# Kernel tuning notes

Measured on AMD Instinct MI355X. Metric: run time of the kernel, lower is better.

Reference implementation:

```python
import jax, jax.numpy as jnp
import numpy as np

N, E, D_IN, H, C = 50000, 1200000, 128, 8, 8  # heads=8, per-head dim=8, hidden=64
EPS_BN = 1e-5


def _bn(x, g, b):
    # BatchNorm1d in training mode: per-feature batch mean / biased var
    m = x.mean(0)
    v = x.var(0)
    return g * (x - m) * jax.lax.rsqrt(v + EPS_BN) + b


def _gatv2(x, src, dst, Wl, Wr, att):
    # PyG GATv2Conv (concat=True, bias=False, negative_slope=0.2, eval-mode dropout)
    xl = (x @ Wl).reshape(N, H, C)  # source transform (lin_l)
    xr = (x @ Wr).reshape(N, H, C)  # target transform (lin_r)
    e = jax.nn.leaky_relu(xl[src] + xr[dst], 0.2)          # [E,H,C]
    logits = jnp.einsum('ehc,hc->eh', e, att)               # [E,H]
    mx = jax.ops.segment_max(logits, dst, num_segments=N)   # [N,H]
    ex = jnp.exp(logits - mx[dst])
    den = jax.ops.segment_sum(ex, dst, num_segments=N)      # [N,H]
    alpha = ex / (den[dst] + 1e-16)                         # segment softmax over in-edges
    msg = xl[src] * alpha[..., None]                        # [E,H,C]
    out = jax.ops.segment_sum(msg.reshape(E, H * C), dst, num_segments=N)
    return out  # [N,64]


def setup_inputs() -> dict:
    key = jax.random.key(0)
    ks = jax.random.split(key, 40)
    d = {}
    d['x'] = jax.random.normal(ks[0], (N, D_IN), dtype=jnp.float32)
    d['edge_index'] = jax.random.randint(ks[1], (2, E), 0, N, dtype=jnp.int64)
    d['Wpre'] = jax.random.normal(ks[2], (D_IN, 64), dtype=jnp.float32) * 0.05
    d['g0'] = jnp.ones((64,), jnp.float32); d['b0'] = jnp.zeros((64,), jnp.float32)
    for i, k0 in zip(range(1, 5), range(3, 19, 4)):
        d[f'Wl{i}'] = jax.random.normal(ks[k0], (64, 64), jnp.float32) * 0.1
        d[f'Wr{i}'] = jax.random.normal(ks[k0 + 1], (64, 64), jnp.float32) * 0.1
        d[f'att{i}'] = jax.random.normal(ks[k0 + 2], (H, C), jnp.float32) * 0.1
        d[f'g{i}'] = jnp.ones((64,), jnp.float32)
        d[f'b{i}'] = jnp.zeros((64,), jnp.float32)
    dims = [64, 48, 32, 16, 2]
    for j in range(4):
        d[f'Wp{j+1}'] = jax.random.normal(ks[20 + j], (dims[j], dims[j + 1]), jnp.float32) * 0.1
        d[f'bp{j+1}'] = jnp.zeros((dims[j + 1],), jnp.float32)
    return d


def reference(x, edge_index, Wpre, g0, b0,
              Wl1, Wr1, att1, g1, b1,
              Wl2, Wr2, att2, g2, b2,
              Wl3, Wr3, att3, g3, b3,
              Wl4, Wr4, att4, g4, b4,
              Wp1, bp1, Wp2, bp2, Wp3, bp3, Wp4, bp4):
    src, dst = edge_index[0], edge_index[1]
    h = jax.nn.elu(_bn(x @ Wpre, g0, b0))
    for Wl, Wr, att, g, b in ((Wl1, Wr1, att1, g1, b1),
                              (Wl2, Wr2, att2, g2, b2),
                              (Wl3, Wr3, att3, g3, b3),
                              (Wl4, Wr4, att4, g4, b4)):
        h = jax.nn.elu(_bn(_gatv2(h, src, dst, Wl, Wr, att) + h, g, b))
    h = jax.nn.elu(h @ Wp1 + bp1)
    h = jax.nn.elu(h @ Wp2 + bp2)
    h = jax.nn.elu(h @ Wp3 + bp3)
    return h @ Wp4 + bp4
```

## Files before the change

### kernel.cpp

```cpp
#include <hip/hip_runtime.h>
#include <hip/hip_bf16.h>
#include <cmath>

__device__ inline void unpack_bf2(unsigned int u, float& lo, float& hi) {
    union { unsigned int i; float f; } a, b;
    a.i = u << 16; b.i = u & 0xffff0000u;
    lo = a.f; hi = b.f;
}
__device__ inline unsigned short bf16_bits(float x) {
    __hip_bfloat16 v = __float2bfloat16(x);
    return *reinterpret_cast<unsigned short*>(&v);
}

template<int K, int M, int ROWS>
__global__ __launch_bounds__(256)
void bn_gemm_kernel(const float* __restrict__ A, const float* __restrict__ B0,
                    const float* __restrict__ B1, float* __restrict__ C,
                    __hip_bfloat16* __restrict__ xlb, __hip_bfloat16* __restrict__ xrb,
                    const float* __restrict__ stats, const float* __restrict__ g,
                    const float* __restrict__ b, int N, float invN)
{
    constexpr int TM  = ROWS * M / 512;
    constexpr int LDA = K + 4;
    constexpr int MT  = M / TM;
    __shared__ float Bs[K * M];
    __shared__ float As[ROWS * LDA];
    __shared__ float sA[K], sB[K];
    if (stats != nullptr && threadIdx.x < K) {
        float m   = stats[threadIdx.x] * invN;
        float var = stats[K + threadIdx.x] * invN - m * m;
        float a   = g[threadIdx.x] * rsqrtf(var + 1e-5f);
        sA[threadIdx.x] = a;
        sB[threadIdx.x] = b[threadIdx.x] - m * a;
    }
    for (int i = threadIdx.x; i < K * M; i += 256) {
        float v;
        if (B1 != nullptr) {
            int k = i / M, m = i - k * M;
            v = (m < M / 2) ? B0[k * (M / 2) + m] : B1[k * (M / 2) + (m - M / 2)];
        } else {
            v = B0[i];
        }
        Bs[i] = v;
    }
    __syncthreads();
    int row0 = blockIdx.x * ROWS;
    for (int i = threadIdx.x; i < ROWS * K; i += 256) {
        int rr = i / K, kk = i - rr * K;
        int r = row0 + rr;
        float v = (r < N) ? A[(size_t)r * K + kk] : 0.f;
        if (stats != nullptr) {
            float t = fmaf(v, sA[kk], sB[kk]);
            v = (t > 0.f) ? t : expm1f(t);
        }
        As[rr * LDA + kk] = v;
    }
    __syncthreads();
    int r0 = (threadIdx.x / MT) * 2;
    int m0 = (threadIdx.x % MT) * TM;
    float acc0[TM], acc1[TM];
    #pragma unroll
    for (int i = 0; i < TM; ++i) { acc0[i] = 0.f; acc1[i] = 0.f; }
    const float* a0p = &As[r0 * LDA];
    const float* a1p = a0p + LDA;
    for (int k = 0; k < K; ++k) {
        float a0 = a0p[k], a1 = a1p[k];
        #pragma unroll
        for (int mm = 0; mm < TM; mm += 4) {
            float4 bv = *(const float4*)&Bs[k * M + m0 + mm];
            acc0[mm + 0] = fmaf(a0, bv.x, acc0[mm + 0]);
            acc0[mm + 1] = fmaf(a0, bv.y, acc0[mm + 1]);
            acc0[mm + 2] = fmaf(a0, bv.z, acc0[mm + 2]);
            acc0[mm + 3] = fmaf(a0, bv.w, acc0[mm + 3]);
            acc1[mm + 0] = fmaf(a1, bv.x, acc1[mm + 0]);
            acc1[mm + 1] = fmaf(a1, bv.y, acc1[mm + 1]);
            acc1[mm + 2] = fmaf(a1, bv.z, acc1[mm + 2]);
            acc1[mm + 3] = fmaf(a1, bv.w, acc1[mm + 3]);
        }
    }
    int rA = row0 + r0, rB = rA + 1;
    if (C != nullptr) {
        #pragma unroll
        for (int mm = 0; mm < TM; mm += 4) {
            if (rA < N)
                *(float4*)&C[(size_t)rA * M + m0 + mm] =
                    make_float4(acc0[mm], acc0[mm+1], acc0[mm+2], acc0[mm+3]);
            if (rB < N)
                *(float4*)&C[(size_t)rB * M + m0 + mm] =
                    make_float4(acc1[mm], acc1[mm+1], acc1[mm+2], acc1[mm+3]);
        }
    } else {
        unsigned int u0[4], u1[4];
        #pragma unroll
        for (int i = 0; i < 4; ++i) {
            u0[i] = (unsigned int)bf16_bits(acc0[2*i]) |
                    ((unsigned int)bf16_bits(acc0[2*i+1]) << 16);
            u1[i] = (unsigned int)bf16_bits(acc1[2*i]) |
                    ((unsigned int)bf16_bits(acc1[2*i+1]) << 16);
        }
        __hip_bfloat16* dst = (m0 < 64) ? xlb : xrb;
        int mo = (m0 < 64) ? m0 : m0 - 64;
        if (rA < N) *(uint4*)(dst + (size_t)rA * 64 + mo) = make_uint4(u0[0],u0[1],u0[2],u0[3]);
        if (rB < N) *(uint4*)(dst + (size_t)rB * 64 + mo) = make_uint4(u1[0],u1[1],u1[2],u1[3]);
    }
}

__global__ __launch_bounds__(256)
void bin_hist_kernel(const int* __restrict__ dsts, int* __restrict__ binCnt, int E)
{
    __shared__ int lh[256];
    lh[threadIdx.x] = 0;
    __syncthreads();
    for (int e = blockIdx.x * 256 + threadIdx.x; e < E; e += gridDim.x * 256)
        atomicAdd(&lh[dsts[e] >> 8], 1);
    __syncthreads();
    if (lh[threadIdx.x] > 0) atomicAdd(&binCnt[threadIdx.x], lh[threadIdx.x]);
}

__global__ __launch_bounds__(256)
void bin_scan_kernel(const int* __restrict__ binCnt, int* __restrict__ binBase,
                     int* __restrict__ binCursor, int* __restrict__ row_ptr,
                     int N, int E)
{
    __shared__ int buf[256];
    int v = binCnt[threadIdx.x];
    buf[threadIdx.x] = v;
    __syncthreads();
    for (int off = 1; off < 256; off <<= 1) {
        int t = (threadIdx.x >= off) ? buf[threadIdx.x - off] : 0;
        __syncthreads();
        buf[threadIdx.x] += t;
        __syncthreads();
    }
    int excl = buf[threadIdx.x] - v;
    binBase[threadIdx.x] = excl;
    binCursor[threadIdx.x] = excl;
    if (threadIdx.x == 255) {
        binBase[256] = buf[255];
        row_ptr[N] = E;
    }
}

#define SCHUNK 4096
__global__ __launch_bounds__(256)
void bin_scatter_kernel(const int* __restrict__ srcs, const int* __restrict__ dsts,
                        int* __restrict__ binCursor, int2* __restrict__ binned, int E)
{
    __shared__ int2 stg[SCHUNK];
    __shared__ int bcnt[256], bexcl[256], bcur[256], gbase[256], sbuf[256];
    int c0 = blockIdx.x * SCHUNK;
    int n = min(SCHUNK, E - c0);
    bcnt[threadIdx.x] = 0;
    __syncthreads();
    for (int k = 0; k < SCHUNK / 256; ++k) {
        int i = c0 + k * 256 + threadIdx.x;
        if (i < E) atomicAdd(&bcnt[dsts[i] >> 8], 1);
    }
    __syncthreads();
    int v = bcnt[threadIdx.x];
    sbuf[threadIdx.x] = v;
    __syncthreads();
    for (int off = 1; off < 256; off <<= 1) {
        int t = (threadIdx.x >= off) ? sbuf[threadIdx.x - off] : 0;
        __syncthreads();
        sbuf[threadIdx.x] += t;
        __syncthreads();
    }
    bexcl[threadIdx.x] = sbuf[threadIdx.x] - v;
    bcur[threadIdx.x]  = sbuf[threadIdx.x] - v;
    __syncthreads();
    for (int k = 0; k < SCHUNK / 256; ++k) {
        int i = c0 + k * 256 + threadIdx.x;
        if (i < E) {
            int s = srcs[i], d = dsts[i];
            int pos = atomicAdd(&bcur[d >> 8], 1);
            stg[pos] = make_int2(s, d);
        }
    }
    __syncthreads();
    gbase[threadIdx.x] = atomicAdd(&binCursor[threadIdx.x], bcnt[threadIdx.x]);
    __syncthreads();
    for (int i = threadIdx.x; i < n; i += 256) {
        int2 p = stg[i];
        int b = p.y >> 8;
        binned[gbase[b] + (i - bexcl[b])] = p;
    }
}

__global__ __launch_bounds__(256)
void bin_finalize_kernel(const int2* __restrict__ binned, const int* __restrict__ binBase,
                         int* __restrict__ row_ptr, int* __restrict__ col, int N)
{
    __shared__ int cnt[256], excl[256], cur[256];
    int b = blockIdx.x;
    int beg = binBase[b], end = binBase[b + 1];
    cnt[threadIdx.x] = 0;
    __syncthreads();
    for (int i = beg + threadIdx.x; i < end; i += 256)
        atomicAdd(&cnt[binned[i].y & 255], 1);
    __syncthreads();
    int v = cnt[threadIdx.x];
    excl[threadIdx.x] = v;
    __syncthreads();
    for (int off = 1; off < 256; off <<= 1) {
        int t = (threadIdx.x >= off) ? excl[threadIdx.x - off] : 0;
        __syncthreads();
        excl[threadIdx.x] += t;
        __syncthreads();
    }
    int ex = excl[threadIdx.x] - v;
    int dstIdx = b * 256 + threadIdx.x;
    if (dstIdx < N) row_ptr[dstIdx] = beg + ex;
    cur[threadIdx.x] = ex;
    __syncthreads();
    for (int i = beg + threadIdx.x; i < end; i += 256) {
        int2 p = binned[i];
        int pos = atomicAdd(&cur[p.y & 255], 1);
        col[beg + pos] = p.x << 7;
    }
}

__device__ inline uint4 ldrow(const char* base_h, int offv, int slot) {
    int off = __shfl(offv, slot);
    return *(const uint4*)(base_h + off);
}

__global__ __launch_bounds__(256)
void gat_node_kernel(const int* __restrict__ row_ptr, const int* __restrict__ coloff,
                     const __hip_bfloat16* __restrict__ xlb,
                     const __hip_bfloat16* __restrict__ xrb,
                     const float* __restrict__ att,
                     const float* __restrict__ zin,
                     const float* __restrict__ stats, const float* __restrict__ g,
                     const float* __restrict__ b,
                     float* __restrict__ zout, float* __restrict__ stats_out,
                     int N, float invN)
{
    int lane = threadIdx.x & 63;
    int wid  = threadIdx.x >> 6;
    int eg   = lane >> 3;
    int h    = lane & 7;

    __shared__ float AB[2][64];
    if (threadIdx.x < 64) {
        float m   = stats[threadIdx.x] * invN;
        float var = stats[64 + threadIdx.x] * invN - m * m;
        float a   = g[threadIdx.x] * rsqrtf(var + 1e-5f);
        AB[0][threadIdx.x] = a;
        AB[1][threadIdx.x] = b[threadIdx.x] - m * a;
    }
    __syncthreads();

    float attv[8];
    {
        const float4* a4 = (const float4*)(att + (h << 3));
        float4 a0 = a4[0], a1 = a4[1];
        attv[0]=a0.x; attv[1]=a0.y; attv[2]=a0.z; attv[3]=a0.w;
        attv[4]=a1.x; attv[5]=a1.y; attv[6]=a1.z; attv[7]=a1.w;
    }
    float fs[8], fs2[8];
    #pragma unroll
    for (int c = 0; c < 8; ++c) { fs[c] = 0.f; fs2[c] = 0.f; }

    const char* xh = (const char*)xlb + (h << 4);
    const int stride = gridDim.x * 4;

    int n = blockIdx.x * 4 + wid;
    int beg = 0, end = 0, cv0 = 0;
    if (n < N) {
        beg = row_ptr[n]; end = row_ptr[n + 1];
        int mm = min(lane, end - beg - 1); if (mm < 0) mm = 0;
        cv0 = coloff[beg + mm];
    }
    while (n < N) {
        uint4 xrp = *(const uint4*)((const char*)xrb + (size_t)n * 128 + (h << 4));
        float xr[8];
        unpack_bf2(xrp.x, xr[0], xr[1]);
        unpack_bf2(xrp.y, xr[2], xr[3]);
        unpack_bf2(xrp.z, xr[4], xr[5]);
        unpack_bf2(xrp.w, xr[6], xr[7]);
        float acc[8];
        #pragma unroll
        for (int c = 0; c < 8; ++c) acc[c] = 0.f;
        float den = 0.f;

        for (int gb = beg; gb < end; gb += 64) {
            int cnt = min(64, end - gb);
            int cv = (gb == beg) ? cv0 : coloff[gb + min(lane, cnt - 1)];
            int nck = (cnt + 15) >> 4;
            uint4 pA = ldrow(xh, cv, min(eg, cnt - 1));
            uint4 pB = ldrow(xh, cv, min(eg + 8, cnt - 1));
            for (int c = 0; c < nck; ++c) {
                uint4 nA = pA, nB = pB;
                if (c + 1 < nck) {
                    nA = ldrow(xh, cv, min((c + 1) * 16 + eg,     cnt - 1));
                    nB = ldrow(xh, cv, min((c + 1) * 16 + 8 + eg, cnt - 1));
                }
                int s0 = c * 16 + eg, s1 = s0 + 8;
                {
                    float xl[8];
                    unpack_bf2(pA.x, xl[0], xl[1]);
                    unpack_bf2(pA.y, xl[2], xl[3]);
                    unpack_bf2(pA.z, xl[4], xl[5]);
                    unpack_bf2(pA.w, xl[6], xl[7]);
                    float logit = 0.f;
                    #pragma unroll
                    for (int cc = 0; cc < 8; ++cc) {
                        float sum = xl[cc] + xr[cc];
                        float lr = fmaxf(sum, 0.2f * sum);
                        logit = fmaf(lr, attv[cc], logit);
                    }
                    float ex = (s0 < cnt) ? __expf(logit) : 0.f;
                    #pragma unroll
                    for (int cc = 0; cc < 8; ++cc) acc[cc] = fmaf(ex, xl[cc], acc[cc]);
                    den += ex;
                }
                {
                    float xl[8];
                    unpack_bf2(pB.x, xl[0], xl[1]);
                    unpack_bf2(pB.y, xl[2], xl[3]);
                    unpack_bf2(pB.z, xl[4], xl[5]);
                    unpack_bf2(pB.w, xl[6], xl[7]);
                    float logit = 0.f;
                    #pragma unroll
                    for (int cc = 0; cc < 8; ++cc) {
                        float sum = xl[cc] + xr[cc];
                        float lr = fmaxf(sum, 0.2f * sum);
                        logit = fmaf(lr, attv[cc], logit);
                    }
                    float ex = (s1 < cnt) ? __expf(logit) : 0.f;
                    #pragma unroll
                    for (int cc = 0; cc < 8; ++cc) acc[cc] = fmaf(ex, xl[cc], acc[cc]);
                    den += ex;
                }
                pA = nA; pB = nB;
            }
        }
        int n2 = n + stride;
        int beg2 = 0, end2 = 0;
        if (n2 < N) { beg2 = row_ptr[n2]; end2 = row_ptr[n2 + 1]; }
        float4 hr0, hr1;
        if (eg == 0) {
            const float4* zp = (const float4*)(zin + (size_t)n * 64 + (h << 3));
            hr0 = zp[0]; hr1 = zp[1];
        }
        #pragma unroll
        for (int off = 8; off <= 32; off <<= 1) {
            den += __shfl_xor(den, off);
            #pragma unroll
            for (int c = 0; c < 8; ++c) acc[c] += __shfl_xor(acc[c], off);
        }
        int cv2 = 0;
        if (n2 < N) {
            int mm = min(lane, end2 - beg2 - 1); if (mm < 0) mm = 0;
            cv2 = coloff[beg2 + mm];
        }
        if (eg == 0) {
            float inv = 1.f / (den + 1e-16f);
            float hraw[8] = {hr0.x, hr0.y, hr0.z, hr0.w, hr1.x, hr1.y, hr1.z, hr1.w};
            float v[8];
            #pragma unroll
            for (int c = 0; c < 8; ++c) {
                int f = (h << 3) + c;
                float t = fmaf(hraw[c], AB[0][f], AB[1][f]);
                float hv = (t > 0.f) ? t : expm1f(t);
                v[c] = fmaf(acc[c], inv, hv);
                fs[c] += v[c];
                fs2[c] += v[c] * v[c];
            }
            float4* z4 = (float4*)(zout + (size_t)n * 64 + (h << 3));
            z4[0] = make_float4(v[0], v[1], v[2], v[3]);
            z4[1] = make_float4(v[4], v[5], v[6], v[7]);
        }
        n = n2; beg = beg2; end = end2; cv0 = cv2;
    }
    __shared__ float lstat[2][4][64];
    if (eg == 0) {
        #pragma unroll
        for (int c = 0; c < 8; ++c) {
            lstat[0][wid][(h << 3) + c] = fs[c];
            lstat[1][wid][(h << 3) + c] = fs2[c];
        }
    }
    __syncthreads();
    if (threadIdx.x < 128) {
        int which = threadIdx.x >> 6;
        int f = threadIdx.x & 63;
        float a = lstat[which][0][f] + lstat[which][1][f] +
                  lstat[which][2][f] + lstat[which][3][f];
        unsafeAtomicAdd(&stats_out[which * 64 + f], a);
    }
}

__global__ __launch_bounds__(256)
void stats_kernel(const float* __restrict__ y, float* __restrict__ stats, int N)
{
    int f  = threadIdx.x & 63;
    int rg = threadIdx.x >> 6;
    float s = 0.f, s2 = 0.f;
    for (int r = blockIdx.x * 4 + rg; r < N; r += gridDim.x * 4) {
        float v = y[(size_t)r * 64 + f];
        s += v;
        s2 += v * v;
    }
    __shared__ float ls[2][4][64];
    ls[0][rg][f] = s;
    ls[1][rg][f] = s2;
    __syncthreads();
    if (threadIdx.x < 128) {
        int which = threadIdx.x >> 6;
        float a = ls[which][0][f] + ls[which][1][f] + ls[which][2][f] + ls[which][3][f];
        unsafeAtomicAdd(&stats[which * 64 + f], a);
    }
}

__global__ __launch_bounds__(256)
void mlp_kernel(const float* __restrict__ z, const float* __restrict__ stats,
                const float* __restrict__ g, const float* __restrict__ b,
                const float* __restrict__ W1, const float* __restrict__ B1,
                const float* __restrict__ W2, const float* __restrict__ B2,
                const float* __restrict__ W3, const float* __restrict__ B3,
                const float* __restrict__ W4, const float* __restrict__ B4,
                float* __restrict__ out, int N, float invN)
{
    __shared__ float w1[64 * 48], w2[48 * 32], w3[32 * 16], w4[16 * 2];
    __shared__ float bb1[48], bb2[32], bb3[16], bb4[2];
    __shared__ float sm[64], sv[64], sg[64], sb[64];
    for (int i = threadIdx.x; i < 64 * 48; i += 256) w1[i] = W1[i];
    for (int i = threadIdx.x; i < 48 * 32; i += 256) w2[i] = W2[i];
    for (int i = threadIdx.x; i < 32 * 16; i += 256) w3[i] = W3[i];
    for (int i = threadIdx.x; i < 16 * 2;  i += 256) w4[i] = W4[i];
    if (threadIdx.x < 48) bb1[threadIdx.x] = B1[threadIdx.x];
    if (threadIdx.x < 32) bb2[threadIdx.x] = B2[threadIdx.x];
    if (threadIdx.x < 16) bb3[threadIdx.x] = B3[threadIdx.x];
    if (threadIdx.x < 2)  bb4[threadIdx.x] = B4[threadIdx.x];
    if (threadIdx.x >= 64 && threadIdx.x < 128) {
        int f = threadIdx.x - 64;
        float m   = stats[f] * invN;
        float var = stats[64 + f] * invN - m * m;
        sm[f] = m;
        sv[f] = rsqrtf(var + 1e-5f);
        sg[f] = g[f];
        sb[f] = b[f];
    }
    __syncthreads();
    int n = blockIdx.x * 256 + threadIdx.x;
    if (n >= N) return;
    float a[64];
    const float4* hp = (const float4*)(z + (size_t)n * 64);
    #pragma unroll
    for (int i = 0; i < 16; ++i) {
        float4 v = hp[i];
        a[4 * i] = v.x; a[4 * i + 1] = v.y; a[4 * i + 2] = v.z; a[4 * i + 3] = v.w;
    }
    #pragma unroll
    for (int k = 0; k < 64; ++k) {
        float t = sg[k] * ((a[k] - sm[k]) * sv[k]) + sb[k];
        a[k] = (t > 0.f) ? t : expm1f(t);
    }
    float t1[48];
    for (int j = 0; j < 48; ++j) {
        float acc = bb1[j];
        #pragma unroll
        for (int k = 0; k < 64; ++k) acc += a[k] * w1[k * 48 + j];
        t1[j] = (acc > 0.f) ? acc : expm1f(acc);
    }
    float t2[32];
    for (int j = 0; j < 32; ++j) {
        float acc = bb2[j];
        #pragma unroll
        for (int k = 0; k < 48; ++k) acc += t1[k] * w2[k * 32 + j];
        t2[j] = (acc > 0.f) ? acc : expm1f(acc);
    }
    float t3[16];
    for (int j = 0; j < 16; ++j) {
        float acc = bb3[j];
        #pragma unroll
        for (int k = 0; k < 32; ++k) acc += t2[k] * w3[k * 16 + j];
        t3[j] = (acc > 0.f) ? acc : expm1f(acc);
    }
    float o0 = bb4[0], o1 = bb4[1];
    #pragma unroll
    for (int k = 0; k < 16; ++k) {
        o0 += t3[k] * w4[k * 2 + 0];
        o1 += t3[k] * w4[k * 2 + 1];
    }
    out[(size_t)n * 2 + 0] = o0;
    out[(size_t)n * 2 + 1] = o1;
}

extern "C" void kernel_launch(void* const* d_in, const int* in_sizes, int n_in,
                              void* d_out, int out_size, void* d_ws, size_t ws_size,
                              hipStream_t stream)
{
    const float* x    = (const float*)d_in[0];
    const int*   ei   = (const int*)d_in[1];
    const float* Wpre = (const float*)d_in[2];
    const float* g0   = (const float*)d_in[3];
    const float* b0   = (const float*)d_in[4];

    const int N = in_sizes[0] / 128;
    const int E = in_sizes[1] / 2;
    const float invN = 1.f / (float)N;
    const int NB = (N + 255) >> 8;

    float* ws  = (float*)d_ws;
    float* zA  = ws;
    float* zB  = zA + (size_t)N * 64;
    __hip_bfloat16* xlb = (__hip_bfloat16*)(zB + (size_t)N * 64);
    __hip_bfloat16* xrb = xlb + (size_t)N * 64;
    float* stats   = (float*)(xrb + (size_t)N * 64);
    int*   row_ptr = (int*)(stats + 5 * 128);
    int*   col     = row_ptr + N + 4;
    int*   binCnt    = col + E + 64;
    int*   binBase   = binCnt + 256;
    int*   binCursor = binBase + 260;
    int2*  binned    = (int2*)zB;

    const int* srcs = ei;
    const int* dsts = ei + E;

    hipMemsetAsync(binCnt, 0, 256 * sizeof(int), stream);
    hipMemsetAsync(stats, 0, 5 * 128 * sizeof(float), stream);
    bin_hist_kernel<<<256, 256, 0, stream>>>(dsts, binCnt, E);
    bin_scan_kernel<<<1, 256, 0, stream>>>(binCnt, binBase, binCursor, row_ptr, N, E);
    bin_scatter_kernel<<<(E + SCHUNK - 1) / SCHUNK, 256, 0, stream>>>(
        srcs, dsts, binCursor, binned, E);
    bin_finalize_kernel<<<NB, 256, 0, stream>>>(binned, binBase, row_ptr, col, N);

    bn_gemm_kernel<128, 64, 32><<<(N + 31) / 32, 256, 0, stream>>>(
        x, Wpre, nullptr, zA, nullptr, nullptr, nullptr, nullptr, nullptr, N, invN);
    stats_kernel<<<1024, 256, 0, stream>>>(zA, stats, N);

    for (int l = 0; l < 4; ++l) {
        const float* Wl  = (const float*)d_in[5 + 5 * l + 0];
        const float* Wr  = (const float*)d_in[5 + 5 * l + 1];
        const float* att = (const float*)d_in[5 + 5 * l + 2];
        const float* gp = (l == 0) ? g0 : (const float*)d_in[5 + 5 * (l - 1) + 3];
        const float* bp = (l == 0) ? b0 : (const float*)d_in[5 + 5 * (l - 1) + 4];
        float* statsp = stats + 128 * l;
        float* zin  = (l & 1) ? zB : zA;
        float* zout = (l & 1) ? zA : zB;

        bn_gemm_kernel<64, 128, 32><<<(N + 31) / 32, 256, 0, stream>>>(
            zin, Wl, Wr, nullptr, xlb, xrb, statsp, gp, bp, N, invN);
        gat_node_kernel<<<2048, 256, 0, stream>>>(
            row_ptr, col, xlb, xrb, att, zin, statsp, gp, bp,
            zout, stats + 128 * (l + 1), N, invN);
    }

    const float* g4  = (const float*)d_in[23];
    const float* b4  = (const float*)d_in[24];
    const float* Wp1 = (const float*)d_in[25]; const float* bp1 = (const float*)d_in[26];
    const float* Wp2 = (const float*)d_in[27]; const float* bp2 = (const float*)d_in[28];
    const float* Wp3 = (const float*)d_in[29]; const float* bp3 = (const float*)d_in[30];
    const float* Wp4 = (const float*)d_in[31]; const float* bp4 = (const float*)d_in[32];
    mlp_kernel<<<(N + 255) / 256, 256, 0, stream>>>(
        zA, stats + 512, g4, b4, Wp1, bp1, Wp2, bp2, Wp3, bp3, Wp4, bp4,
        (float*)d_out, N, invN);
}
```

Before: 598.1 us.

## Pack binned edges into 32-bit words and use 8-edge groups with triple-buffered prefetch

The binning stage now packs src and dst into one 32-bit word (src in the high 16 bits, dst in the low 16) instead of an int2. This halves the shared-memory staging and the global traffic for the binned edge array. The GAT node kernel's inner loop changes from 16-edge chunks with double-buffered loads to 8-edge groups with a three-deep rolling prefetch, which cuts wasted work on padded edges for low-degree nodes. The packing assumes node indices fit in 16 bits, but N is 50000, so dst fits and the dst>>8 bin indices stay intact. Source indices of 65536 or more cannot occur because N<65536, so the packing is safe for this size but is not general.

```diff
diff --git a/kernel.cpp b/kernel.cpp
--- a/kernel.cpp
+++ b/kernel.cpp
@@ -144,9 +144,10 @@
 #define SCHUNK 4096
 __global__ __launch_bounds__(256)
 void bin_scatter_kernel(const int* __restrict__ srcs, const int* __restrict__ dsts,
-                        int* __restrict__ binCursor, int2* __restrict__ binned, int E)
-{
-    __shared__ int2 stg[SCHUNK];
+                        int* __restrict__ binCursor, unsigned int* __restrict__ binned,
+                        int E)
+{
+    __shared__ unsigned int stg[SCHUNK];
     __shared__ int bcnt[256], bexcl[256], bcur[256], gbase[256], sbuf[256];
     int c0 = blockIdx.x * SCHUNK;
     int n = min(SCHUNK, E - c0);
@@ -172,23 +173,24 @@
     for (int k = 0; k < SCHUNK / 256; ++k) {
         int i = c0 + k * 256 + threadIdx.x;
         if (i < E) {
-            int s = srcs[i], d = dsts[i];
+            unsigned int s = (unsigned int)srcs[i], d = (unsigned int)dsts[i];
             int pos = atomicAdd(&bcur[d >> 8], 1);
-            stg[pos] = make_int2(s, d);
+            stg[pos] = (s << 16) | d;
         }
     }
     __syncthreads();
     gbase[threadIdx.x] = atomicAdd(&binCursor[threadIdx.x], bcnt[threadIdx.x]);
     __syncthreads();
     for (int i = threadIdx.x; i < n; i += 256) {
-        int2 p = stg[i];
-        int b = p.y >> 8;
+        unsigned int p = stg[i];
+        int b = (p & 0xFFFFu) >> 8;
         binned[gbase[b] + (i - bexcl[b])] = p;
     }
 }
 
 __global__ __launch_bounds__(256)
-void bin_finalize_kernel(const int2* __restrict__ binned, const int* __restrict__ binBase,
+void bin_finalize_kernel(const unsigned int* __restrict__ binned,
+                         const int* __restrict__ binBase,
                          int* __restrict__ row_ptr, int* __restrict__ col, int N)
 {
     __shared__ int cnt[256], excl[256], cur[256];
@@ -197,7 +199,7 @@
     cnt[threadIdx.x] = 0;
     __syncthreads();
     for (int i = beg + threadIdx.x; i < end; i += 256)
-        atomicAdd(&cnt[binned[i].y & 255], 1);
+        atomicAdd(&cnt[binned[i] & 255u], 1);
     __syncthreads();
     int v = cnt[threadIdx.x];
     excl[threadIdx.x] = v;
@@ -214,9 +216,9 @@
     cur[threadIdx.x] = ex;
     __syncthreads();
     for (int i = beg + threadIdx.x; i < end; i += 256) {
-        int2 p = binned[i];
-        int pos = atomicAdd(&cur[p.y & 255], 1);
-        col[beg + pos] = p.x << 7;
+        unsigned int p = binned[i];
+        int pos = atomicAdd(&cur[p & 255u], 1);
+        col[beg + pos] = (int)(p >> 16) << 7;
     }
 }
 
@@ -286,54 +288,33 @@
 
         for (int gb = beg; gb < end; gb += 64) {
             int cnt = min(64, end - gb);
-            int cv = (gb == beg) ? cv0 : coloff[gb + min(lane, cnt - 1)];
-            int nck = (cnt + 15) >> 4;
-            uint4 pA = ldrow(xh, cv, min(eg, cnt - 1));
-            uint4 pB = ldrow(xh, cv, min(eg + 8, cnt - 1));
-            for (int c = 0; c < nck; ++c) {
-                uint4 nA = pA, nB = pB;
-                if (c + 1 < nck) {
-                    nA = ldrow(xh, cv, min((c + 1) * 16 + eg,     cnt - 1));
-                    nB = ldrow(xh, cv, min((c + 1) * 16 + 8 + eg, cnt - 1));
+            int cm1 = cnt - 1;
+            int cv = (gb == beg) ? cv0 : coloff[gb + min(lane, cm1)];
+            int ng = (cnt + 7) >> 3;
+            uint4 qa = ldrow(xh, cv, min(eg, cm1));
+            uint4 qb = (ng > 1) ? ldrow(xh, cv, min(8 + eg, cm1))  : qa;
+            uint4 qc = (ng > 2) ? ldrow(xh, cv, min(16 + eg, cm1)) : qb;
+            for (int i = 0; i < ng; ++i) {
+                int s = i * 8 + eg;
+                float xl[8];
+                unpack_bf2(qa.x, xl[0], xl[1]);
+                unpack_bf2(qa.y, xl[2], xl[3]);
+                unpack_bf2(qa.z, xl[4], xl[5]);
+                unpack_bf2(qa.w, xl[6], xl[7]);
+                qa = qb; qb = qc;
+                if (i + 3 < ng)
+                    qc = ldrow(xh, cv, min((i + 3) * 8 + eg, cm1));
+                float logit = 0.f;
+                #pragma unroll
+                for (int cc = 0; cc < 8; ++cc) {
+                    float sum = xl[cc] + xr[cc];
+                    float lr = fmaxf(sum, 0.2f * sum);
+                    logit = fmaf(lr, attv[cc], logit);
                 }
-                int s0 = c * 16 + eg, s1 = s0 + 8;
-                {
-                    float xl[8];
-                    unpack_bf2(pA.x, xl[0], xl[1]);
-                    unpack_bf2(pA.y, xl[2], xl[3]);
-                    unpack_bf2(pA.z, xl[4], xl[5]);
-                    unpack_bf2(pA.w, xl[6], xl[7]);
-                    float logit = 0.f;
-                    #pragma unroll
-                    for (int cc = 0; cc < 8; ++cc) {
-                        float sum = xl[cc] + xr[cc];
-                        float lr = fmaxf(sum, 0.2f * sum);
-                        logit = fmaf(lr, attv[cc], logit);
-                    }
-                    float ex = (s0 < cnt) ? __expf(logit) : 0.f;
-                    #pragma unroll
-                    for (int cc = 0; cc < 8; ++cc) acc[cc] = fmaf(ex, xl[cc], acc[cc]);
-                    den += ex;
-                }
-                {
-                    float xl[8];
-                    unpack_bf2(pB.x, xl[0], xl[1]);
-                    unpack_bf2(pB.y, xl[2], xl[3]);
-                    unpack_bf2(pB.z, xl[4], xl[5]);
-                    unpack_bf2(pB.w, xl[6], xl[7]);
-                    float logit = 0.f;
-                    #pragma unroll
-                    for (int cc = 0; cc < 8; ++cc) {
-                        float sum = xl[cc] + xr[cc];
-                        float lr = fmaxf(sum, 0.2f * sum);
-                        logit = fmaf(lr, attv[cc], logit);
-                    }
-                    float ex = (s1 < cnt) ? __expf(logit) : 0.f;
-                    #pragma unroll
-                    for (int cc = 0; cc < 8; ++cc) acc[cc] = fmaf(ex, xl[cc], acc[cc]);
-                    den += ex;
-                }
-                pA = nA; pB = nB;
+                float ex = (s < cnt) ? __expf(logit) : 0.f;
+                #pragma unroll
+                for (int cc = 0; cc < 8; ++cc) acc[cc] = fmaf(ex, xl[cc], acc[cc]);
+                den += ex;
             }
         }
         int n2 = n + stride;
@@ -515,7 +496,7 @@
     int*   binCnt    = col + E + 64;
     int*   binBase   = binCnt + 256;
     int*   binCursor = binBase + 260;
-    int2*  binned    = (int2*)zB;
+    unsigned int* binned = (unsigned int*)zB;
 
     const int* srcs = ei;
     const int* dsts = ei + E;
```

After: 625.4 us. 4.6% more time.

## Split GAT aggregation into two head-half passes over separate xl tables

Applied to the files above, without the earlier changes.

The source-feature table xl is split into two half-width bf16 arrays (heads 0-3 and heads 4-7, 64 bytes per row each). The GAT node kernel now runs as two passes, each gathering only one half, so the randomly gathered working set per pass is half the size and more likely to stay cache-resident. Binned edges are also packed into a single 32-bit word (src<<16 | dst), which halves the binning traffic but only holds for node ids below 65536. In exchange, CSR traversal, the xr/zin loads and the launch overhead are paid twice per layer.

```diff
diff --git a/kernel.cpp b/kernel.cpp
--- a/kernel.cpp
+++ b/kernel.cpp
@@ -16,7 +16,8 @@
 __global__ __launch_bounds__(256)
 void bn_gemm_kernel(const float* __restrict__ A, const float* __restrict__ B0,
                     const float* __restrict__ B1, float* __restrict__ C,
-                    __hip_bfloat16* __restrict__ xlb, __hip_bfloat16* __restrict__ xrb,
+                    __hip_bfloat16* __restrict__ xlA, __hip_bfloat16* __restrict__ xlB,
+                    __hip_bfloat16* __restrict__ xrb,
                     const float* __restrict__ stats, const float* __restrict__ g,
                     const float* __restrict__ b, int N, float invN)
 {
@@ -98,10 +99,13 @@
             u1[i] = (unsigned int)bf16_bits(acc1[2*i]) |
                     ((unsigned int)bf16_bits(acc1[2*i+1]) << 16);
         }
-        __hip_bfloat16* dst = (m0 < 64) ? xlb : xrb;
-        int mo = (m0 < 64) ? m0 : m0 - 64;
-        if (rA < N) *(uint4*)(dst + (size_t)rA * 64 + mo) = make_uint4(u0[0],u0[1],u0[2],u0[3]);
-        if (rB < N) *(uint4*)(dst + (size_t)rB * 64 + mo) = make_uint4(u1[0],u1[1],u1[2],u1[3]);
+        __hip_bfloat16* dst;
+        int mo, str;
+        if (m0 < 32)      { dst = xlA; mo = m0;      str = 32; }
+        else if (m0 < 64) { dst = xlB; mo = m0 - 32; str = 32; }
+        else              { dst = xrb; mo = m0 - 64; str = 64; }
+        if (rA < N) *(uint4*)(dst + (size_t)rA * str + mo) = make_uint4(u0[0],u0[1],u0[2],u0[3]);
+        if (rB < N) *(uint4*)(dst + (size_t)rB * str + mo) = make_uint4(u1[0],u1[1],u1[2],u1[3]);
     }
 }
 
@@ -144,9 +148,10 @@
 #define SCHUNK 4096
 __global__ __launch_bounds__(256)
 void bin_scatter_kernel(const int* __restrict__ srcs, const int* __restrict__ dsts,
-                        int* __restrict__ binCursor, int2* __restrict__ binned, int E)
-{
-    __shared__ int2 stg[SCHUNK];
+                        int* __restrict__ binCursor, unsigned int* __restrict__ binned,
+                        int E)
+{
+    __shared__ unsigned int stg[SCHUNK];
     __shared__ int bcnt[256], bexcl[256], bcur[256], gbase[256], sbuf[256];
     int c0 = blockIdx.x * SCHUNK;
     int n = min(SCHUNK, E - c0);
@@ -172,23 +177,24 @@
     for (int k = 0; k < SCHUNK / 256; ++k) {
         int i = c0 + k * 256 + threadIdx.x;
         if (i < E) {
-            int s = srcs[i], d = dsts[i];
+            unsigned int s = (unsigned int)srcs[i], d = (unsigned int)dsts[i];
             int pos = atomicAdd(&bcur[d >> 8], 1);
-            stg[pos] = make_int2(s, d);
+            stg[pos] = (s << 16) | d;
         }
     }
     __syncthreads();
     gbase[threadIdx.x] = atomicAdd(&binCursor[threadIdx.x], bcnt[threadIdx.x]);
     __syncthreads();
     for (int i = threadIdx.x; i < n; i += 256) {
-        int2 p = stg[i];
-        int b = p.y >> 8;
+        unsigned int p = stg[i];
+        int b = (p & 0xFFFFu) >> 8;
         binned[gbase[b] + (i - bexcl[b])] = p;
     }
 }
 
 __global__ __launch_bounds__(256)
-void bin_finalize_kernel(const int2* __restrict__ binned, const int* __restrict__ binBase,
+void bin_finalize_kernel(const unsigned int* __restrict__ binned,
+                         const int* __restrict__ binBase,
                          int* __restrict__ row_ptr, int* __restrict__ col, int N)
 {
     __shared__ int cnt[256], excl[256], cur[256];
@@ -197,7 +203,7 @@
     cnt[threadIdx.x] = 0;
     __syncthreads();
     for (int i = beg + threadIdx.x; i < end; i += 256)
-        atomicAdd(&cnt[binned[i].y & 255], 1);
+        atomicAdd(&cnt[binned[i] & 255u], 1);
     __syncthreads();
     int v = cnt[threadIdx.x];
     excl[threadIdx.x] = v;
@@ -214,9 +220,9 @@
     cur[threadIdx.x] = ex;
     __syncthreads();
     for (int i = beg + threadIdx.x; i < end; i += 256) {
-        int2 p = binned[i];
-        int pos = atomicAdd(&cur[p.y & 255], 1);
-        col[beg + pos] = p.x << 7;
+        unsigned int p = binned[i];
+        int pos = atomicAdd(&cur[p & 255u], 1);
+        col[beg + pos] = (int)(p >> 16) << 6;
     }
 }
 
@@ -225,9 +231,10 @@
     return *(const uint4*)(base_h + off);
 }
 
-__global__ __launch_bounds__(256)
-void gat_node_kernel(const int* __restrict__ row_ptr, const int* __restrict__ coloff,
-                     const __hip_bfloat16* __restrict__ xlb,
+template<int PASS>
+__global__ __launch_bounds__(256)
+void gat_pass_kernel(const int* __restrict__ row_ptr, const int* __restrict__ coloff,
+                     const __hip_bfloat16* __restrict__ xlt,
                      const __hip_bfloat16* __restrict__ xrb,
                      const float* __restrict__ att,
                      const float* __restrict__ zin,
@@ -238,8 +245,9 @@
 {
     int lane = threadIdx.x & 63;
     int wid  = threadIdx.x >> 6;
-    int eg   = lane >> 3;
-    int h    = lane & 7;
+    int eg   = lane >> 2;
+    int h4   = lane & 3;
+    int hh   = (PASS << 2) + h4;
 
     __shared__ float AB[2][64];
     if (threadIdx.x < 64) {
@@ -253,7 +261,7 @@
 
     float attv[8];
     {
-        const float4* a4 = (const float4*)(att + (h << 3));
+        const float4* a4 = (const float4*)(att + (hh << 3));
         float4 a0 = a4[0], a1 = a4[1];
         attv[0]=a0.x; attv[1]=a0.y; attv[2]=a0.z; attv[3]=a0.w;
         attv[4]=a1.x; attv[5]=a1.y; attv[6]=a1.z; attv[7]=a1.w;
@@ -262,7 +270,7 @@
     #pragma unroll
     for (int c = 0; c < 8; ++c) { fs[c] = 0.f; fs2[c] = 0.f; }
 
-    const char* xh = (const char*)xlb + (h << 4);
+    const char* xh = (const char*)xlt + (h4 << 4);
     const int stride = gridDim.x * 4;
 
     int n = blockIdx.x * 4 + wid;
@@ -273,7 +281,7 @@
         cv0 = coloff[beg + mm];
     }
     while (n < N) {
-        uint4 xrp = *(const uint4*)((const char*)xrb + (size_t)n * 128 + (h << 4));
+        uint4 xrp = *(const uint4*)((const char*)xrb + (size_t)n * 128 + (hh << 4));
         float xr[8];
         unpack_bf2(xrp.x, xr[0], xr[1]);
         unpack_bf2(xrp.y, xr[2], xr[3]);
@@ -286,17 +294,18 @@
 
         for (int gb = beg; gb < end; gb += 64) {
             int cnt = min(64, end - gb);
-            int cv = (gb == beg) ? cv0 : coloff[gb + min(lane, cnt - 1)];
-            int nck = (cnt + 15) >> 4;
-            uint4 pA = ldrow(xh, cv, min(eg, cnt - 1));
-            uint4 pB = ldrow(xh, cv, min(eg + 8, cnt - 1));
+            int cm1 = cnt - 1;
+            int cv = (gb == beg) ? cv0 : coloff[gb + min(lane, cm1)];
+            int nck = (cnt + 31) >> 5;
+            uint4 pA = ldrow(xh, cv, min(eg, cm1));
+            uint4 pB = ldrow(xh, cv, min(16 + eg, cm1));
             for (int c = 0; c < nck; ++c) {
                 uint4 nA = pA, nB = pB;
                 if (c + 1 < nck) {
-                    nA = ldrow(xh, cv, min((c + 1) * 16 + eg,     cnt - 1));
-                    nB = ldrow(xh, cv, min((c + 1) * 16 + 8 + eg, cnt - 1));
+                    nA = ldrow(xh, cv, min((c + 1) * 32 + eg,      cm1));
+                    nB = ldrow(xh, cv, min((c + 1) * 32 + 16 + eg, cm1));
                 }
-                int s0 = c * 16 + eg, s1 = s0 + 8;
+                int s0 = c * 32 + eg, s1 = s0 + 16;
                 {
                     float xl[8];
                     unpack_bf2(pA.x, xl[0], xl[1]);
@@ -341,11 +350,11 @@
         if (n2 < N) { beg2 = row_ptr[n2]; end2 = row_ptr[n2 + 1]; }
         float4 hr0, hr1;
         if (eg == 0) {
-            const float4* zp = (const float4*)(zin + (size_t)n * 64 + (h << 3));
+            const float4* zp = (const float4*)(zin + (size_t)n * 64 + (hh << 3));
             hr0 = zp[0]; hr1 = zp[1];
         }
         #pragma unroll
-        for (int off = 8; off <= 32; off <<= 1) {
+        for (int off = 4; off <= 32; off <<= 1) {
             den += __shfl_xor(den, off);
             #pragma unroll
             for (int c = 0; c < 8; ++c) acc[c] += __shfl_xor(acc[c], off);
@@ -361,34 +370,34 @@
             float v[8];
             #pragma unroll
             for (int c = 0; c < 8; ++c) {
-                int f = (h << 3) + c;
+                int f = (hh << 3) + c;
                 float t = fmaf(hraw[c], AB[0][f], AB[1][f]);
                 float hv = (t > 0.f) ? t : expm1f(t);
                 v[c] = fmaf(acc[c], inv, hv);
                 fs[c] += v[c];
                 fs2[c] += v[c] * v[c];
             }
-            float4* z4 = (float4*)(zout + (size_t)n * 64 + (h << 3));
+            float4* z4 = (float4*)(zout + (size_t)n * 64 + (hh << 3));
             z4[0] = make_float4(v[0], v[1], v[2], v[3]);
             z4[1] = make_float4(v[4], v[5], v[6], v[7]);
         }
         n = n2; beg = beg2; end = end2; cv0 = cv2;
     }
-    __shared__ float lstat[2][4][64];
+    __shared__ float lstat[2][4][32];
     if (eg == 0) {
         #pragma unroll
         for (int c = 0; c < 8; ++c) {
-            lstat[0][wid][(h << 3) + c] = fs[c];
-            lstat[1][wid][(h << 3) + c] = fs2[c];
-        }
-    }
-    __syncthreads();
-    if (threadIdx.x < 128) {
-        int which = threadIdx.x >> 6;
-        int f = threadIdx.x & 63;
-        float a = lstat[which][0][f] + lstat[which][1][f] +
-                  lstat[which][2][f] + lstat[which][3][f];
-        unsafeAtomicAdd(&stats_out[which * 64 + f], a);
+            lstat[0][wid][(h4 << 3) + c] = fs[c];
+            lstat[1][wid][(h4 << 3) + c] = fs2[c];
+        }
+    }
+    __syncthreads();
+    if (threadIdx.x < 64) {
+        int which = threadIdx.x >> 5;
+        int fl = threadIdx.x & 31;
+        float a = lstat[which][0][fl] + lstat[which][1][fl] +
+                  lstat[which][2][fl] + lstat[which][3][fl];
+        unsafeAtomicAdd(&stats_out[which * 64 + (PASS << 5) + fl], a);
     }
 }
 
@@ -507,15 +516,16 @@
     float* ws  = (float*)d_ws;
     float* zA  = ws;
     float* zB  = zA + (size_t)N * 64;
-    __hip_bfloat16* xlb = (__hip_bfloat16*)(zB + (size_t)N * 64);
-    __hip_bfloat16* xrb = xlb + (size_t)N * 64;
+    __hip_bfloat16* xlA = (__hip_bfloat16*)(zB + (size_t)N * 64);
+    __hip_bfloat16* xlB = xlA + (size_t)N * 32;
+    __hip_bfloat16* xrb = xlB + (size_t)N * 32;
     float* stats   = (float*)(xrb + (size_t)N * 64);
     int*   row_ptr = (int*)(stats + 5 * 128);
     int*   col     = row_ptr + N + 4;
     int*   binCnt    = col + E + 64;
     int*   binBase   = binCnt + 256;
     int*   binCursor = binBase + 260;
-    int2*  binned    = (int2*)zB;
+    unsigned int* binned = (unsigned int*)zB;
 
     const int* srcs = ei;
     const int* dsts = ei + E;
@@ -529,7 +539,8 @@
     bin_finalize_kernel<<<NB, 256, 0, stream>>>(binned, binBase, row_ptr, col, N);
 
     bn_gemm_kernel<128, 64, 32><<<(N + 31) / 32, 256, 0, stream>>>(
-        x, Wpre, nullptr, zA, nullptr, nullptr, nullptr, nullptr, nullptr, N, invN);
+        x, Wpre, nullptr, zA, nullptr, nullptr, nullptr, nullptr, nullptr, nullptr,
+        N, invN);
     stats_kernel<<<1024, 256, 0, stream>>>(zA, stats, N);
 
     for (int l = 0; l < 4; ++l) {
@@ -543,9 +554,12 @@
         float* zout = (l & 1) ? zA : zB;
 
         bn_gemm_kernel<64, 128, 32><<<(N + 31) / 32, 256, 0, stream>>>(
-            zin, Wl, Wr, nullptr, xlb, xrb, statsp, gp, bp, N, invN);
-        gat_node_kernel<<<2048, 256, 0, stream>>>(
-            row_ptr, col, xlb, xrb, att, zin, statsp, gp, bp,
+            zin, Wl, Wr, nullptr, xlA, xlB, xrb, statsp, gp, bp, N, invN);
+        gat_pass_kernel<0><<<2048, 256, 0, stream>>>(
+            row_ptr, col, xlA, xrb, att, zin, statsp, gp, bp,
+            zout, stats + 128 * (l + 1), N, invN);
+        gat_pass_kernel<1><<<2048, 256, 0, stream>>>(
+            row_ptr, col, xlB, xrb, att, zin, statsp, gp, bp,
             zout, stats + 128 * (l + 1), N, invN);
     }
 
```

Result: slower. 722.9 us (+20.9%).
